# Performance work log

Hardware: AMD Instinct MI355X
Metric: run time of the kernel (lower is better)

## Reference

```python
import jax, jax.numpy as jnp
import numpy as np

F_DIM = 64; HID = 64; HEADS = 2; DH = 32; NG = 4; EPS = 1e-5; SCALE = 8.0  # sqrt(hid_dim)
B = 4; H = 64; W = 64; S = 8; CIN = 64


def _ln(x, g, b):
    mu = x.mean(-1, keepdims=True)
    var = ((x - mu) ** 2).mean(-1, keepdims=True)
    return (x - mu) * jax.lax.rsqrt(var + EPS) * g + b


def _gn(x, g, b):
    # x: [b, C, H, W]; normalize per group over (C/NG, H, W)
    bb, c, hh, ww = x.shape
    xg = x.reshape(bb, NG, -1)
    mu = xg.mean(-1, keepdims=True)
    var = ((xg - mu) ** 2).mean(-1, keepdims=True)
    xn = ((xg - mu) * jax.lax.rsqrt(var + EPS)).reshape(bb, c, hh, ww)
    return xn * g[None, :, None, None] + b[None, :, None, None]


def _mha(xq, xkv, qw, qb, kw, kb, vw, vb, ow, ob):
    # per-head attention with scaling by sqrt(hid_dim) (as in the source)
    q = xq @ qw + qb
    k = xkv @ kw + kb
    v = xkv @ vw + vb
    bb, l, _ = q.shape
    m = k.shape[1]
    qh = q.reshape(bb, l, HEADS, DH)
    kh = k.reshape(bb, m, HEADS, DH)
    vh = v.reshape(bb, m, HEADS, DH)
    s = jnp.einsum('blhd,bmhd->bhlm', qh, kh) / SCALE
    p = jax.nn.softmax(s, axis=-1)
    z = jnp.einsum('bhlm,bmhd->blhd', p, vh).reshape(bb, l, HID)
    return z @ ow + ob


def setup_inputs() -> dict:
    key = jax.random.key(0)
    ks = jax.random.split(key, 34)
    p = lambda k, shp: (jax.random.normal(k, shp, jnp.float32) * 0.02)
    d = {
        'x': jax.random.normal(ks[0], (B, H, W, F_DIM), jnp.float32),
        'slots': jax.random.normal(ks[1], (B, S, CIN), jnp.float32),
        'conv1_w': p(ks[2], (F_DIM, F_DIM)), 'conv1_b': p(ks[3], (F_DIM,)),
        'conv2_w': p(ks[4], (F_DIM, F_DIM)), 'conv2_b': p(ks[5], (F_DIM,)),
        'gn_g': jnp.ones((F_DIM,), jnp.float32), 'gn_b': jnp.zeros((F_DIM,), jnp.float32),
        'ln2_g': jnp.ones((F_DIM,), jnp.float32), 'ln2_b': jnp.zeros((F_DIM,), jnp.float32),
        'ln3_g': jnp.ones((F_DIM,), jnp.float32), 'ln3_b': jnp.zeros((F_DIM,), jnp.float32),
        'ln4_g': jnp.ones((F_DIM,), jnp.float32), 'ln4_b': jnp.zeros((F_DIM,), jnp.float32),
        'sa_qw': p(ks[6], (F_DIM, HID)), 'sa_qb': p(ks[7], (HID,)),
        'sa_kw': p(ks[8], (F_DIM, HID)), 'sa_kb': p(ks[9], (HID,)),
        'sa_vw': p(ks[10], (F_DIM, HID)), 'sa_vb': p(ks[11], (HID,)),
        'sa_ow': p(ks[12], (HID, F_DIM)), 'sa_ob': p(ks[13], (F_DIM,)),
        'ca_qw': p(ks[14], (F_DIM, HID)), 'ca_qb': p(ks[15], (HID,)),
        'ca_kw': p(ks[16], (CIN, HID)), 'ca_kb': p(ks[17], (HID,)),
        'ca_vw': p(ks[18], (CIN, HID)), 'ca_vb': p(ks[19], (HID,)),
        'ca_ow': p(ks[20], (HID, F_DIM)), 'ca_ob': p(ks[21], (F_DIM,)),
        'ff1_w': p(ks[22], (F_DIM, F_DIM)), 'ff1_b': p(ks[23], (F_DIM,)),
    }
    return d


def reference(x, slots, conv1_w, conv1_b, conv2_w, conv2_b, gn_g, gn_b,
              ln2_g, ln2_b, ln3_g, ln3_b, ln4_g, ln4_b,
              sa_qw, sa_qb, sa_kw, sa_kb, sa_vw, sa_vb, sa_ow, sa_ob,
              ca_qw, ca_qb, ca_kw, ca_kb, ca_vw, ca_vb, ca_ow, ca_ob,
              ff1_w, ff1_b):
    b, h, w, f = x.shape
    xc = jnp.transpose(x, (0, 3, 1, 2))               # [b,f,h,w]
    xc = _gn(xc, gn_g, gn_b)
    xc = jnp.einsum('bchw,oc->bohw', xc, conv1_w) + conv1_b[None, :, None, None]
    # faithful to torch: .contiguous().view(b,-1,f) on channels-first layout
    xs = xc.reshape(b, h * w, f)
    # repeat = 1
    xs = jax.nn.gelu(_ln(_mha(xs, xs, sa_qw, sa_qb, sa_kw, sa_kb, sa_vw, sa_vb, sa_ow, sa_ob), ln2_g, ln2_b) + xs, approximate=False)
    xs = _ln(_mha(xs, slots, ca_qw, ca_qb, ca_kw, ca_kb, ca_vw, ca_vb, ca_ow, ca_ob), ln3_g, ln3_b) + xs
    xs = _ln(xs @ ff1_w + ff1_b, ln4_g, ln4_b) + xs
    xo = jnp.transpose(xs.reshape(b, h, w, f), (0, 3, 1, 2))
    xo = jnp.einsum('bchw,oc->bohw', xo, conv2_w) + conv2_b[None, :, None, None]
    return jnp.transpose(xo, (0, 2, 3, 1))
```

## Files before the change

### kernel.cpp

```cpp
#include <hip/hip_runtime.h>
#include <hip/hip_bf16.h>
#include <math.h>

#define NBATCH 4
#define LTOK   4096
#define FD     64
#define KSPLIT 8
#define MBLK   16

typedef __attribute__((ext_vector_type(8))) short short8v;
typedef __attribute__((ext_vector_type(4))) float f32x4;
typedef __attribute__((ext_vector_type(16))) float f32x16;

static __device__ inline uint32_t packbf2(float a, float b) {
    float2 f; f.x = a; f.y = b;
    __hip_bfloat162 h = __float22bfloat162_rn(f);
    uint32_t u; __builtin_memcpy(&u, &h, 4);
    return u;
}
static __device__ inline ushort packbf1(float a) {
    __hip_bfloat16 h = __float2bfloat16(a);
    ushort u; __builtin_memcpy(&u, &h, 2);
    return u;
}
static __device__ inline float gelu_exact(float y) {
    return 0.5f * y * (1.0f + erff(y * 0.70710678118654752f));
}

__global__ void gn_part_kernel(const float* __restrict__ x,
                               float* __restrict__ partS, float* __restrict__ partSS) {
    const int b = blockIdx.x >> 6, c = blockIdx.x & 63;
    const int t = threadIdx.x, l = t & 63, wv = t >> 6;
    const float4* xb = (const float4*)(x + (size_t)b * 262144) + (size_t)c * 1024;
    float s = 0.f, ss = 0.f;
#pragma unroll
    for (int k = 0; k < 4; k++) {
        float4 v = xb[t + 256 * k];
        s += (v.x + v.y) + (v.z + v.w);
        ss += (v.x * v.x + v.y * v.y) + (v.z * v.z + v.w * v.w);
    }
#pragma unroll
    for (int o = 0; o < 4; o++) {
        const int off = (int[]){1, 2, 16, 32}[o];
        s += __shfl_xor(s, off, 64);
        ss += __shfl_xor(ss, off, 64);
    }
    __shared__ float ls_s[4][4], ls_ss[4][4];
    if ((l & 51) == 0) { ls_s[wv][(l >> 2) & 3] = s; ls_ss[wv][(l >> 2) & 3] = ss; }
    __syncthreads();
    if (t < 4) {
        float S = 0.f, SS = 0.f;
#pragma unroll
        for (int w2 = 0; w2 < 4; w2++) { S += ls_s[w2][t]; SS += ls_ss[w2][t]; }
        partS[b * 256 + t * 64 + c] = S;
        partSS[b * 256 + t * 64 + c] = SS;
    }
}

__global__ void gn_conv1_kernel(const float* __restrict__ x,
                                const float* __restrict__ partS, const float* __restrict__ partSS,
                                const float* __restrict__ gg, const float* __restrict__ gb,
                                const float* __restrict__ w, const float* __restrict__ bias,
                                float* __restrict__ out) {
    const int b = blockIdx.x >> 6, i = blockIdx.x & 63;
    const int t = threadIdx.x;
    __shared__ float xn[64][65];
    __shared__ float wsm[64][64];
    __shared__ float sm[4], sr[4];
    {
        float sv = partS[b * 256 + t];
        float ssv = partSS[b * 256 + t];
        for (int o = 32; o; o >>= 1) { sv += __shfl_xor(sv, o, 64); ssv += __shfl_xor(ssv, o, 64); }
        if ((t & 63) == 0) {
            float mean = sv * (1.f / 65536.f);
            float var = ssv * (1.f / 65536.f) - mean * mean;
            sm[t >> 6] = mean;
            sr[t >> 6] = rsqrtf(var + 1e-5f);
        }
    }
    __syncthreads();
    {
        const int j = t >> 2, c0 = (t & 3) * 16, g = c0 >> 4;
        const float mean = sm[g], rstd = sr[g];
        const float* src = x + (((size_t)b * 64 + i) * 64 + j) * 64 + c0;
#pragma unroll
        for (int k = 0; k < 4; k++) {
            float4 v = *(const float4*)(src + 4 * k);
            xn[j][c0 + 4 * k + 0] = (v.x - mean) * rstd * gg[c0 + 4 * k + 0] + gb[c0 + 4 * k + 0];
            xn[j][c0 + 4 * k + 1] = (v.y - mean) * rstd * gg[c0 + 4 * k + 1] + gb[c0 + 4 * k + 1];
            xn[j][c0 + 4 * k + 2] = (v.z - mean) * rstd * gg[c0 + 4 * k + 2] + gb[c0 + 4 * k + 2];
            xn[j][c0 + 4 * k + 3] = (v.w - mean) * rstd * gg[c0 + 4 * k + 3] + gb[c0 + 4 * k + 3];
        }
        const int o = t >> 2, cc0 = (t & 3) * 16;
#pragma unroll
        for (int k = 0; k < 16; k++) wsm[cc0 + k][o] = w[o * 64 + cc0 + k];
    }
    __syncthreads();
    const int jj = t & 63, olo = (t >> 6) * 16;
    float acc[16];
#pragma unroll
    for (int oi = 0; oi < 16; oi++) acc[oi] = bias[olo + oi];
    for (int c = 0; c < 64; c++) {
        float xv = xn[jj][c];
#pragma unroll
        for (int oi = 0; oi < 16; oi++) acc[oi] += xv * wsm[c][olo + oi];
    }
#pragma unroll
    for (int oi = 0; oi < 16; oi++)
        out[((size_t)b * LTOK + (size_t)(olo + oi) * 64 + i) * 64 + jj] = acc[oi];
}

__global__ void qkv_kernel(const float* __restrict__ in,
                           const float* __restrict__ qw, const float* __restrict__ qb,
                           const float* __restrict__ kw, const float* __restrict__ kb,
                           const float* __restrict__ vw, const float* __restrict__ vb,
                           ushort* __restrict__ Qo, ushort* __restrict__ KF, ushort* __restrict__ VF) {
    __shared__ float xt[64][68];
    __shared__ float wt[64][64];
    __shared__ ushort vtr[64 * 72];
    const int t = threadIdx.x;
    const int ph = blockIdx.y;
    const size_t tok0 = (size_t)blockIdx.x * 64;
    const int b = blockIdx.x >> 6;
    const int tokb0 = (blockIdx.x & 63) * 64;
    const int r = t >> 2, cq = t & 3, olo = cq * 16;
    const float* W = (ph == 0) ? qw : (ph == 1) ? kw : vw;
    const float* Bb = (ph == 0) ? qb : (ph == 1) ? kb : vb;
    {
        const float4* src = (const float4*)(in + tok0 * 64) + (size_t)t * 4;
        float4* dst = (float4*)&xt[r][olo];
#pragma unroll
        for (int k = 0; k < 4; k++) dst[k] = src[k];
        const float4* ws2 = (const float4*)W + (size_t)t * 4;
        float4* wd = (float4*)wt + (size_t)t * 4;
#pragma unroll
        for (int k = 0; k < 4; k++) wd[k] = ws2[k];
    }
    __syncthreads();
    float acc[16];
#pragma unroll
    for (int k = 0; k < 4; k++) {
        float4 bv = *(const float4*)(Bb + olo + 4 * k);
        acc[4 * k] = bv.x; acc[4 * k + 1] = bv.y; acc[4 * k + 2] = bv.z; acc[4 * k + 3] = bv.w;
    }
    for (int f = 0; f < 64; f++) {
        float xv = xt[r][f];
#pragma unroll
        for (int oi = 0; oi < 16; oi++) acc[oi] += xv * wt[f][olo + oi];
    }
    if (ph == 0) {
        const float sc = 0.180336880111f;
        uint32_t u[8];
#pragma unroll
        for (int i = 0; i < 8; i++) u[i] = packbf2(acc[2 * i] * sc, acc[2 * i + 1] * sc);
        ushort* op = Qo + (tok0 + r) * 64 + olo;
        *(uint4*)op = make_uint4(u[0], u[1], u[2], u[3]);
        *(uint4*)(op + 8) = make_uint4(u[4], u[5], u[6], u[7]);
    } else if (ph == 1) {
        uint32_t u[8];
#pragma unroll
        for (int i = 0; i < 8; i++) u[i] = packbf2(acc[2 * i], acc[2 * i + 1]);
        const int tokb = tokb0 + r;
        const int m = tokb >> 5, tq = tokb & 31;
        const int hh = cq >> 1, f = cq & 1;
        const int bhh = b * 2 + hh;
        ushort* p0 = KF + ((size_t)(bhh * 128 + m) * 2 + f) * 512;
        *(uint4*)(p0 + tq * 8)        = make_uint4(u[0], u[1], u[2], u[3]);
        *(uint4*)(p0 + (32 + tq) * 8) = make_uint4(u[4], u[5], u[6], u[7]);
    } else {
#pragma unroll
        for (int oi = 0; oi < 16; oi++) vtr[(olo + oi) * 72 + r] = packbf1(acc[oi]);
        __syncthreads();
        const int o = t >> 2, ch = t & 3;
        const int lq2 = o & 31, hh = o >> 5, bhh = b * 2 + hh;
        const int m = (tokb0 >> 5) + (ch >> 1), f = ch & 1;
        uint4 a0 = *(const uint4*)&vtr[o * 72 + ch * 16];
        uint4 a1 = *(const uint4*)&vtr[o * 72 + ch * 16 + 8];
        ushort* p0 = VF + ((size_t)(bhh * 128 + m) * 2 + f) * 512;
        *(uint4*)(p0 + lq2 * 8)        = a0;
        *(uint4*)(p0 + (32 + lq2) * 8) = a1;
    }
}

__global__ __launch_bounds__(256, 4) void flash_mfma(const ushort* __restrict__ Q,
                                                     const ushort* __restrict__ KF,
                                                     const ushort* __restrict__ VF,
                                                     ushort* __restrict__ ZpAll,
                                                     float* __restrict__ Ls) {
    const int qt = blockIdx.x;
    const int bh = blockIdx.y;
    const int ks = blockIdx.z;
    const int b = bh >> 1, h = bh & 1;
    const int t = threadIdx.x;
    const int w = t >> 6, l = t & 63, lq = l & 31, sig = l >> 5;

    const size_t base = (size_t)b * LTOK * 64 + h * 32;
    const int q0 = qt * 256 + w * 64;

    const ushort* qp = Q + base + (size_t)(q0 + lq) * 64 + 8 * sig;
    const short8v qfA0 = *(const short8v*)(qp);
    const short8v qfA1 = *(const short8v*)(qp + 16);
    const short8v qfB0 = *(const short8v*)(qp + 32 * 64);
    const short8v qfB1 = *(const short8v*)(qp + 32 * 64 + 16);

    const ushort* kfp = KF + ((size_t)(bh * 128 + ks * MBLK) * 2) * 512 + l * 8;
    const ushort* vfp = VF + ((size_t)(bh * 128 + ks * MBLK) * 2) * 512 + l * 8;

    f32x16 accA, accB, zero16;
#pragma unroll
    for (int i = 0; i < 16; i++) { accA[i] = 0.f; accB[i] = 0.f; zero16[i] = 0.f; }
    float laccA = 0.f, laccB = 0.f;

    auto mk_aP = [&](const f32x16& st, float& lacc, short8v& aP0v, short8v& aP1v) {
        uint32_t pk[8];
#pragma unroll
        for (int i = 0; i < 8; i++) {
            float p0 = __builtin_amdgcn_exp2f(st[2 * i]);
            float p1 = __builtin_amdgcn_exp2f(st[2 * i + 1]);
            lacc += p0 + p1;
            pk[i] = packbf2(p0, p1);
        }
        uint32_t w0 = pk[0], w2 = pk[2], w1 = pk[1], w3 = pk[3];
        uint32_t x0 = pk[4], x2 = pk[6], x1 = pk[5], x3 = pk[7];
        asm volatile("v_permlane32_swap_b32 %0, %1" : "+v"(w0), "+v"(w2));
        asm volatile("v_permlane32_swap_b32 %0, %1" : "+v"(w1), "+v"(w3));
        asm volatile("v_permlane32_swap_b32 %0, %1" : "+v"(x0), "+v"(x2));
        asm volatile("v_permlane32_swap_b32 %0, %1" : "+v"(x1), "+v"(x3));
        uint4 A0 = make_uint4(w0, w1, w2, w3), A1 = make_uint4(x0, x1, x2, x3);
        __builtin_memcpy(&aP0v, &A0, 16);
        __builtin_memcpy(&aP1v, &A1, 16);
    };

#pragma unroll 4
    for (int m = 0; m < MBLK; m++) {
        const short8v kf0 = *(const short8v*)kfp;
        const short8v kf1 = *(const short8v*)(kfp + 512);
        const short8v vf0 = *(const short8v*)vfp;
        const short8v vf1 = *(const short8v*)(vfp + 512);
        kfp += 1024; vfp += 1024;

        f32x16 st = __builtin_amdgcn_mfma_f32_32x32x16_bf16(kf0, qfA0, zero16, 0, 0, 0);
        st = __builtin_amdgcn_mfma_f32_32x32x16_bf16(kf1, qfA1, st, 0, 0, 0);
        short8v aPA0, aPA1;
        mk_aP(st, laccA, aPA0, aPA1);

        f32x16 st2 = __builtin_amdgcn_mfma_f32_32x32x16_bf16(kf0, qfB0, zero16, 0, 0, 0);
        st2 = __builtin_amdgcn_mfma_f32_32x32x16_bf16(kf1, qfB1, st2, 0, 0, 0);
        short8v aPB0, aPB1;
        mk_aP(st2, laccB, aPB0, aPB1);

        accA = __builtin_amdgcn_mfma_f32_32x32x16_bf16(aPA0, vf0, accA, 0, 0, 0);
        accA = __builtin_amdgcn_mfma_f32_32x32x16_bf16(aPA1, vf1, accA, 0, 0, 0);
        accB = __builtin_amdgcn_mfma_f32_32x32x16_bf16(aPB0, vf0, accB, 0, 0, 0);
        accB = __builtin_amdgcn_mfma_f32_32x32x16_bf16(aPB1, vf1, accB, 0, 0, 0);
    }

    ushort* Zo = ZpAll + (size_t)ks * (NBATCH * LTOK * FD);
#pragma unroll
    for (int r = 0; r < 16; r++) {
        const int qr = q0 + (r & 3) + 8 * (r >> 2) + 4 * sig;
        Zo[base + (size_t)qr * 64 + lq] = packbf1(accA[r]);
        Zo[base + (size_t)(qr + 32) * 64 + lq] = packbf1(accB[r]);
    }
    laccA += __shfl_xor(laccA, 32, 64);
    laccB += __shfl_xor(laccB, 32, 64);
    if (l < 32) {
        Ls[ks * 32768 + bh * 4096 + q0 + lq] = laccA;
        Ls[ks * 32768 + bh * 4096 + q0 + 32 + lq] = laccB;
    }
}

__global__ __launch_bounds__(256) void tail_fused(
    const ushort* __restrict__ ZpAll,
    const float* __restrict__ Ls, const float* __restrict__ xs0,
    const float* __restrict__ slots,
    const float* __restrict__ ckw, const float* __restrict__ ckb,
    const float* __restrict__ cvw, const float* __restrict__ cvb,
    const float* __restrict__ ow, const float* __restrict__ ob,
    const float* __restrict__ g2, const float* __restrict__ b2,
    const float* __restrict__ qw, const float* __restrict__ qb,
    const float* __restrict__ cow, const float* __restrict__ cob,
    const float* __restrict__ g3, const float* __restrict__ b3,
    const float* __restrict__ fw, const float* __restrict__ fb,
    const float* __restrict__ g4, const float* __restrict__ b4,
    const float* __restrict__ cw, const float* __restrict__ cb,
    float* __restrict__ out)
{
    const int t = threadIdx.x;
    const size_t tok0 = (size_t)blockIdx.x * 32;
    const int b = blockIdx.x >> 7;
    const int r = t >> 3, c = t & 7, olo = c * 8;
    __shared__ float xt[32][68];
    __shared__ float wt[64][64];
    __shared__ float kcs[512], vcs[512], sls[512];

    float acc[8], res[8];

    auto stage_w = [&](const float* W) {
#pragma unroll
        for (int k = 0; k < 4; k++)
            ((float4*)wt)[4 * t + k] = ((const float4*)W)[4 * t + k];
    };
    auto stage_x_res = [&]() {
        float4* xd = (float4*)&xt[r][olo];
        xd[0] = make_float4(res[0], res[1], res[2], res[3]);
        xd[1] = make_float4(res[4], res[5], res[6], res[7]);
    };
    auto load8 = [&](float* dst, const float* p) {
        float4 u0 = *(const float4*)(p + olo);
        float4 u1 = *(const float4*)(p + olo + 4);
        dst[0] = u0.x; dst[1] = u0.y; dst[2] = u0.z; dst[3] = u0.w;
        dst[4] = u1.x; dst[5] = u1.y; dst[6] = u1.z; dst[7] = u1.w;
    };
    auto mm = [&](const float* bias) {
        load8(acc, bias);
        for (int f = 0; f < 64; f++) {
            float xv = xt[r][f];
#pragma unroll
            for (int oi = 0; oi < 8; oi++) acc[oi] += xv * wt[f][olo + oi];
        }
    };
    auto ln = [&](const float* gv, const float* bv, bool dogelu) {
        float s1 = 0.f, s2 = 0.f;
#pragma unroll
        for (int oi = 0; oi < 8; oi++) { s1 += acc[oi]; s2 += acc[oi] * acc[oi]; }
#pragma unroll
        for (int o = 1; o <= 4; o <<= 1) {
            s1 += __shfl_xor(s1, o, 64);
            s2 += __shfl_xor(s2, o, 64);
        }
        float mean = s1 * (1.f / 64.f);
        float var = s2 * (1.f / 64.f) - mean * mean;
        float rstd = rsqrtf(var + 1e-5f);
        float gl[8], bl[8];
        load8(gl, gv); load8(bl, bv);
#pragma unroll
        for (int oi = 0; oi < 8; oi++) {
            float y = (acc[oi] - mean) * rstd * gl[oi] + bl[oi] + res[oi];
            res[oi] = dogelu ? gelu_exact(y) : y;
        }
    };

    {
        if (t < 128) ((float4*)sls)[t] = ((const float4*)(slots + (size_t)b * 512))[t];
        float zs[8];
#pragma unroll
        for (int j = 0; j < 8; j++) zs[j] = 0.f;
#pragma unroll
        for (int kb = 0; kb < KSPLIT; kb++) {
            const uint4 u = *(const uint4*)(ZpAll + (size_t)kb * (NBATCH * LTOK * FD)
                                            + tok0 * 64 + (size_t)t * 8);
            const uint32_t arr[4] = {u.x, u.y, u.z, u.w};
#pragma unroll
            for (int j = 0; j < 4; j++) {
                zs[2 * j]     += __uint_as_float(arr[j] << 16);
                zs[2 * j + 1] += __uint_as_float(arr[j] & 0xffff0000u);
            }
        }
        const int hh = olo >> 5;
        const int bh_ = b * 2 + hh;
        const int tokb = (blockIdx.x & 127) * 32 + r;
        float lt = 0.f;
#pragma unroll
        for (int kb = 0; kb < KSPLIT; kb++) lt += Ls[kb * 32768 + bh_ * 4096 + tokb];
        const float inv = 1.0f / lt;
        float4* xd = (float4*)&xt[r][olo];
        xd[0] = make_float4(zs[0] * inv, zs[1] * inv, zs[2] * inv, zs[3] * inv);
        xd[1] = make_float4(zs[4] * inv, zs[5] * inv, zs[6] * inv, zs[7] * inv);
        stage_w(ow);
        float4 r0 = *(const float4*)(xs0 + (tok0 + r) * 64 + olo);
        float4 r1 = *(const float4*)(xs0 + (tok0 + r) * 64 + olo + 4);
        res[0] = r0.x; res[1] = r0.y; res[2] = r0.z; res[3] = r0.w;
        res[4] = r1.x; res[5] = r1.y; res[6] = r1.z; res[7] = r1.w;
    }
    __syncthreads();
    for (int jo = t; jo < 512; jo += 256) {
        const int j = jo >> 6, o = jo & 63;
        float ak = ckb[o], av = cvb[o];
#pragma unroll 8
        for (int c2 = 0; c2 < 64; c2++) {
            float sv = sls[j * 64 + c2];
            ak += sv * ckw[c2 * 64 + o];
            av += sv * cvw[c2 * 64 + o];
        }
        kcs[jo] = ak; vcs[jo] = av;
    }
    mm(ob);
    ln(g2, b2, true);

    __syncthreads();
    stage_x_res();
    stage_w(qw);
    __syncthreads();
    mm(qb);
    {
        float p[8];
        float mx = -3.0e38f;
#pragma unroll
        for (int j = 0; j < 8; j++) {
            float d = 0.f;
#pragma unroll
            for (int i2 = 0; i2 < 8; i2++) d += acc[i2] * kcs[j * 64 + olo + i2];
            d += __shfl_xor(d, 1, 64);
            d += __shfl_xor(d, 2, 64);
            d *= 0.125f;
            p[j] = d;
            mx = fmaxf(mx, d);
        }
        float es = 0.f;
#pragma unroll
        for (int j = 0; j < 8; j++) { p[j] = __expf(p[j] - mx); es += p[j]; }
        float inv = 1.f / es;
#pragma unroll
        for (int oi = 0; oi < 8; oi++) {
            float z = 0.f;
#pragma unroll
            for (int j = 0; j < 8; j++) z += p[j] * vcs[j * 64 + olo + oi];
            acc[oi] = z * inv;
        }
    }

    __syncthreads();
    {
        float4* xd = (float4*)&xt[r][olo];
        xd[0] = make_float4(acc[0], acc[1], acc[2], acc[3]);
        xd[1] = make_float4(acc[4], acc[5], acc[6], acc[7]);
    }
    stage_w(cow);
    __syncthreads();
    mm(cob);
    ln(g3, b3, false);

    __syncthreads();
    stage_x_res();
    stage_w(fw);
    __syncthreads();
    mm(fb);
    ln(g4, b4, false);

    __syncthreads();
    stage_x_res();
    {
        const int o5 = t >> 2, c5 = (t & 3) * 16;
#pragma unroll
        for (int k = 0; k < 16; k++) wt[c5 + k][o5] = cw[o5 * 64 + c5 + k];
    }
    __syncthreads();
    mm(cb);
    float* op = out + (tok0 + r) * 64 + olo;
    *(float4*)op = make_float4(acc[0], acc[1], acc[2], acc[3]);
    *(float4*)(op + 4) = make_float4(acc[4], acc[5], acc[6], acc[7]);
}

extern "C" void kernel_launch(void* const* d_in, const int* in_sizes, int n_in,
                              void* d_out, int out_size, void* d_ws, size_t ws_size,
                              hipStream_t stream) {
    const float* x       = (const float*)d_in[0];
    const float* slots   = (const float*)d_in[1];
    const float* conv1_w = (const float*)d_in[2];
    const float* conv1_b = (const float*)d_in[3];
    const float* conv2_w = (const float*)d_in[4];
    const float* conv2_b = (const float*)d_in[5];
    const float* gn_g    = (const float*)d_in[6];
    const float* gn_b    = (const float*)d_in[7];
    const float* ln2_g   = (const float*)d_in[8];
    const float* ln2_b   = (const float*)d_in[9];
    const float* ln3_g   = (const float*)d_in[10];
    const float* ln3_b   = (const float*)d_in[11];
    const float* ln4_g   = (const float*)d_in[12];
    const float* ln4_b   = (const float*)d_in[13];
    const float* sa_qw   = (const float*)d_in[14];
    const float* sa_qb   = (const float*)d_in[15];
    const float* sa_kw   = (const float*)d_in[16];
    const float* sa_kb   = (const float*)d_in[17];
    const float* sa_vw   = (const float*)d_in[18];
    const float* sa_vb   = (const float*)d_in[19];
    const float* sa_ow   = (const float*)d_in[20];
    const float* sa_ob   = (const float*)d_in[21];
    const float* ca_qw   = (const float*)d_in[22];
    const float* ca_qb   = (const float*)d_in[23];
    const float* ca_kw   = (const float*)d_in[24];
    const float* ca_kb   = (const float*)d_in[25];
    const float* ca_vw   = (const float*)d_in[26];
    const float* ca_vb   = (const float*)d_in[27];
    const float* ca_ow   = (const float*)d_in[28];
    const float* ca_ob   = (const float*)d_in[29];
    const float* ff1_w   = (const float*)d_in[30];
    const float* ff1_b   = (const float*)d_in[31];

    float* ws = (float*)d_ws;
    const size_t NBUF = (size_t)NBATCH * LTOK * FD;
    float* partS  = ws;
    float* partSS = ws + 1024;
    float* A      = ws + 4096;
    ushort* KF    = (ushort*)(A + NBUF);
    ushort* VF    = KF + NBUF;
    ushort* Qb    = VF + NBUF;
    ushort* ZpAll = Qb + NBUF;
    float* Ls     = (float*)(ZpAll + (size_t)KSPLIT * NBUF);

    gn_part_kernel<<<256, 256, 0, stream>>>(x, partS, partSS);
    gn_conv1_kernel<<<256, 256, 0, stream>>>(x, partS, partSS, gn_g, gn_b, conv1_w, conv1_b, A);
    qkv_kernel<<<dim3(256, 3), 256, 0, stream>>>(A, sa_qw, sa_qb, sa_kw, sa_kb, sa_vw, sa_vb, Qb, KF, VF);
    flash_mfma<<<dim3(16, 8, KSPLIT), 256, 0, stream>>>(Qb, KF, VF, ZpAll, Ls);
    tail_fused<<<512, 256, 0, stream>>>(ZpAll, Ls, A, slots,
                                        ca_kw, ca_kb, ca_vw, ca_vb,
                                        sa_ow, sa_ob, ln2_g, ln2_b,
                                        ca_qw, ca_qb, ca_ow, ca_ob, ln3_g, ln3_b,
                                        ff1_w, ff1_b, ln4_g, ln4_b,
                                        conv2_w, conv2_b, (float*)d_out);
}
```

Baseline: 88.25 us.

## Precompute cross-attn slot K/V once, merge QKV phases, widen small kernels

The cross-attention K/V projection of the slots moves out of tail_fused, where all 512 blocks recomputed it, into one extra block of the GN partial-sum kernel that writes it to workspace. The QKV kernel now computes Q, K and V in one block of 512 threads instead of three separate grid-y phases, loading the input tile once. gn_conv1 also goes to 512 threads with 8 outputs per thread. The extra K/V block is serial within one block and may lengthen the first kernel, and the larger blocks raise register and LDS pressure.

```diff
diff --git a/kernel.cpp b/kernel.cpp
--- a/kernel.cpp
+++ b/kernel.cpp
@@ -28,9 +28,28 @@
 }
 
 __global__ void gn_part_kernel(const float* __restrict__ x,
-                               float* __restrict__ partS, float* __restrict__ partSS) {
+                               const float* __restrict__ slots,
+                               const float* __restrict__ ckw, const float* __restrict__ ckb,
+                               const float* __restrict__ cvw, const float* __restrict__ cvb,
+                               float* __restrict__ partS, float* __restrict__ partSS,
+                               float* __restrict__ kvca) {
+    const int t = threadIdx.x;
+    if (blockIdx.x == 256) {
+        __shared__ float sl[2048];
+        for (int i = t; i < 2048; i += 256) sl[i] = slots[i];
+        __syncthreads();
+        for (int idx = t; idx < 4096; idx += 256) {
+            int which = idx >> 11, rem = idx & 2047, bj = rem >> 6, o = rem & 63;
+            const float* W = which ? cvw : ckw;
+            const float* Bb = which ? cvb : ckb;
+            float acc = Bb[o];
+            for (int c = 0; c < 64; c++) acc += sl[bj * 64 + c] * W[c * 64 + o];
+            kvca[idx] = acc;
+        }
+        return;
+    }
     const int b = blockIdx.x >> 6, c = blockIdx.x & 63;
-    const int t = threadIdx.x, l = t & 63, wv = t >> 6;
+    const int l = t & 63, wv = t >> 6;
     const float4* xb = (const float4*)(x + (size_t)b * 262144) + (size_t)c * 1024;
     float s = 0.f, ss = 0.f;
 #pragma unroll
@@ -57,17 +76,18 @@
     }
 }
 
-__global__ void gn_conv1_kernel(const float* __restrict__ x,
-                                const float* __restrict__ partS, const float* __restrict__ partSS,
-                                const float* __restrict__ gg, const float* __restrict__ gb,
-                                const float* __restrict__ w, const float* __restrict__ bias,
-                                float* __restrict__ out) {
+__global__ __launch_bounds__(512) void gn_conv1_kernel(
+    const float* __restrict__ x,
+    const float* __restrict__ partS, const float* __restrict__ partSS,
+    const float* __restrict__ gg, const float* __restrict__ gb,
+    const float* __restrict__ w, const float* __restrict__ bias,
+    float* __restrict__ out) {
     const int b = blockIdx.x >> 6, i = blockIdx.x & 63;
     const int t = threadIdx.x;
     __shared__ float xn[64][65];
     __shared__ float wsm[64][64];
     __shared__ float sm[4], sr[4];
-    {
+    if (t < 256) {
         float sv = partS[b * 256 + t];
         float ssv = partSS[b * 256 + t];
         for (int o = 32; o; o >>= 1) { sv += __shfl_xor(sv, o, 64); ssv += __shfl_xor(ssv, o, 64); }
@@ -80,105 +100,108 @@
     }
     __syncthreads();
     {
-        const int j = t >> 2, c0 = (t & 3) * 16, g = c0 >> 4;
+        const int j = t >> 3, c0 = (t & 7) * 8, g = c0 >> 4;
         const float mean = sm[g], rstd = sr[g];
         const float* src = x + (((size_t)b * 64 + i) * 64 + j) * 64 + c0;
-#pragma unroll
-        for (int k = 0; k < 4; k++) {
-            float4 v = *(const float4*)(src + 4 * k);
-            xn[j][c0 + 4 * k + 0] = (v.x - mean) * rstd * gg[c0 + 4 * k + 0] + gb[c0 + 4 * k + 0];
-            xn[j][c0 + 4 * k + 1] = (v.y - mean) * rstd * gg[c0 + 4 * k + 1] + gb[c0 + 4 * k + 1];
-            xn[j][c0 + 4 * k + 2] = (v.z - mean) * rstd * gg[c0 + 4 * k + 2] + gb[c0 + 4 * k + 2];
-            xn[j][c0 + 4 * k + 3] = (v.w - mean) * rstd * gg[c0 + 4 * k + 3] + gb[c0 + 4 * k + 3];
-        }
-        const int o = t >> 2, cc0 = (t & 3) * 16;
-#pragma unroll
-        for (int k = 0; k < 16; k++) wsm[cc0 + k][o] = w[o * 64 + cc0 + k];
-    }
-    __syncthreads();
-    const int jj = t & 63, olo = (t >> 6) * 16;
-    float acc[16];
-#pragma unroll
-    for (int oi = 0; oi < 16; oi++) acc[oi] = bias[olo + oi];
+        float4 v0 = *(const float4*)src;
+        float4 v1 = *(const float4*)(src + 4);
+        float vv[8] = {v0.x, v0.y, v0.z, v0.w, v1.x, v1.y, v1.z, v1.w};
+#pragma unroll
+        for (int k = 0; k < 8; k++)
+            xn[j][c0 + k] = (vv[k] - mean) * rstd * gg[c0 + k] + gb[c0 + k];
+        const int o = t >> 3, cc0 = (t & 7) * 8;
+#pragma unroll
+        for (int k = 0; k < 8; k++) wsm[cc0 + k][o] = w[o * 64 + cc0 + k];
+    }
+    __syncthreads();
+    const int jj = t & 63, og = t >> 6;
+    const int olo = og * 8;
+    float acc[8];
+#pragma unroll
+    for (int oi = 0; oi < 8; oi++) acc[oi] = bias[olo + oi];
     for (int c = 0; c < 64; c++) {
         float xv = xn[jj][c];
-#pragma unroll
-        for (int oi = 0; oi < 16; oi++) acc[oi] += xv * wsm[c][olo + oi];
-    }
-#pragma unroll
-    for (int oi = 0; oi < 16; oi++)
+        float4 w0 = *(const float4*)&wsm[c][olo];
+        float4 w1 = *(const float4*)&wsm[c][olo + 4];
+        acc[0] += xv * w0.x; acc[1] += xv * w0.y; acc[2] += xv * w0.z; acc[3] += xv * w0.w;
+        acc[4] += xv * w1.x; acc[5] += xv * w1.y; acc[6] += xv * w1.z; acc[7] += xv * w1.w;
+    }
+#pragma unroll
+    for (int oi = 0; oi < 8; oi++)
         out[((size_t)b * LTOK + (size_t)(olo + oi) * 64 + i) * 64 + jj] = acc[oi];
 }
 
-__global__ void qkv_kernel(const float* __restrict__ in,
-                           const float* __restrict__ qw, const float* __restrict__ qb,
-                           const float* __restrict__ kw, const float* __restrict__ kb,
-                           const float* __restrict__ vw, const float* __restrict__ vb,
-                           ushort* __restrict__ Qo, ushort* __restrict__ KF, ushort* __restrict__ VF) {
+__global__ __launch_bounds__(512) void qkv_kernel(
+    const float* __restrict__ in,
+    const float* __restrict__ qw, const float* __restrict__ qb,
+    const float* __restrict__ kw, const float* __restrict__ kb,
+    const float* __restrict__ vw, const float* __restrict__ vb,
+    ushort* __restrict__ Qo, ushort* __restrict__ KF, ushort* __restrict__ VF) {
     __shared__ float xt[64][68];
-    __shared__ float wt[64][64];
+    __shared__ float wq[64][64], wk2[64][64], wv2[64][64];
     __shared__ ushort vtr[64 * 72];
     const int t = threadIdx.x;
-    const int ph = blockIdx.y;
     const size_t tok0 = (size_t)blockIdx.x * 64;
     const int b = blockIdx.x >> 6;
     const int tokb0 = (blockIdx.x & 63) * 64;
-    const int r = t >> 2, cq = t & 3, olo = cq * 16;
-    const float* W = (ph == 0) ? qw : (ph == 1) ? kw : vw;
-    const float* Bb = (ph == 0) ? qb : (ph == 1) ? kb : vb;
-    {
-        const float4* src = (const float4*)(in + tok0 * 64) + (size_t)t * 4;
-        float4* dst = (float4*)&xt[r][olo];
-#pragma unroll
-        for (int k = 0; k < 4; k++) dst[k] = src[k];
-        const float4* ws2 = (const float4*)W + (size_t)t * 4;
-        float4* wd = (float4*)wt + (size_t)t * 4;
-#pragma unroll
-        for (int k = 0; k < 4; k++) wd[k] = ws2[k];
-    }
-    __syncthreads();
-    float acc[16];
-#pragma unroll
-    for (int k = 0; k < 4; k++) {
-        float4 bv = *(const float4*)(Bb + olo + 4 * k);
-        acc[4 * k] = bv.x; acc[4 * k + 1] = bv.y; acc[4 * k + 2] = bv.z; acc[4 * k + 3] = bv.w;
-    }
-    for (int f = 0; f < 64; f++) {
-        float xv = xt[r][f];
-#pragma unroll
-        for (int oi = 0; oi < 16; oi++) acc[oi] += xv * wt[f][olo + oi];
-    }
-    if (ph == 0) {
+    {
+        const float4* src = (const float4*)(in + tok0 * 64) + 2 * t;
+        float* dst = &xt[t >> 3][(t & 7) * 8];
+        *(float4*)dst = src[0];
+        *(float4*)(dst + 4) = src[1];
+        ((float4*)wq)[2 * t] = ((const float4*)qw)[2 * t];
+        ((float4*)wq)[2 * t + 1] = ((const float4*)qw)[2 * t + 1];
+        ((float4*)wk2)[2 * t] = ((const float4*)kw)[2 * t];
+        ((float4*)wk2)[2 * t + 1] = ((const float4*)kw)[2 * t + 1];
+        ((float4*)wv2)[2 * t] = ((const float4*)vw)[2 * t];
+        ((float4*)wv2)[2 * t + 1] = ((const float4*)vw)[2 * t + 1];
+    }
+    __syncthreads();
+    const int r2 = t >> 3, fo = (t & 7) * 8;
+    const int tokb = tokb0 + r2;
+
+    auto proj = [&](const float (*W)[64], const float* Bb, float* acc) {
+        float4 b0 = *(const float4*)(Bb + fo);
+        float4 b1 = *(const float4*)(Bb + fo + 4);
+        acc[0] = b0.x; acc[1] = b0.y; acc[2] = b0.z; acc[3] = b0.w;
+        acc[4] = b1.x; acc[5] = b1.y; acc[6] = b1.z; acc[7] = b1.w;
+        for (int f = 0; f < 64; f++) {
+            float xv = xt[r2][f];
+            float4 w0 = *(const float4*)&W[f][fo];
+            float4 w1 = *(const float4*)&W[f][fo + 4];
+            acc[0] += xv * w0.x; acc[1] += xv * w0.y; acc[2] += xv * w0.z; acc[3] += xv * w0.w;
+            acc[4] += xv * w1.x; acc[5] += xv * w1.y; acc[6] += xv * w1.z; acc[7] += xv * w1.w;
+        }
+    };
+
+    float acc[8];
+    proj(wq, qb, acc);
+    {
         const float sc = 0.180336880111f;
-        uint32_t u[8];
-#pragma unroll
-        for (int i = 0; i < 8; i++) u[i] = packbf2(acc[2 * i] * sc, acc[2 * i + 1] * sc);
-        ushort* op = Qo + (tok0 + r) * 64 + olo;
-        *(uint4*)op = make_uint4(u[0], u[1], u[2], u[3]);
-        *(uint4*)(op + 8) = make_uint4(u[4], u[5], u[6], u[7]);
-    } else if (ph == 1) {
-        uint32_t u[8];
-#pragma unroll
-        for (int i = 0; i < 8; i++) u[i] = packbf2(acc[2 * i], acc[2 * i + 1]);
-        const int tokb = tokb0 + r;
+        uint4 u = make_uint4(packbf2(acc[0] * sc, acc[1] * sc), packbf2(acc[2] * sc, acc[3] * sc),
+                             packbf2(acc[4] * sc, acc[5] * sc), packbf2(acc[6] * sc, acc[7] * sc));
+        *(uint4*)(Qo + (tok0 + r2) * 64 + fo) = u;
+    }
+    proj(wk2, kb, acc);
+    {
+        uint4 u = make_uint4(packbf2(acc[0], acc[1]), packbf2(acc[2], acc[3]),
+                             packbf2(acc[4], acc[5]), packbf2(acc[6], acc[7]));
         const int m = tokb >> 5, tq = tokb & 31;
-        const int hh = cq >> 1, f = cq & 1;
+        const int hh = fo >> 5, rem = fo & 31, ff = rem >> 4, sg = (rem >> 3) & 1;
         const int bhh = b * 2 + hh;
-        ushort* p0 = KF + ((size_t)(bhh * 128 + m) * 2 + f) * 512;
-        *(uint4*)(p0 + tq * 8)        = make_uint4(u[0], u[1], u[2], u[3]);
-        *(uint4*)(p0 + (32 + tq) * 8) = make_uint4(u[4], u[5], u[6], u[7]);
-    } else {
-#pragma unroll
-        for (int oi = 0; oi < 16; oi++) vtr[(olo + oi) * 72 + r] = packbf1(acc[oi]);
-        __syncthreads();
-        const int o = t >> 2, ch = t & 3;
-        const int lq2 = o & 31, hh = o >> 5, bhh = b * 2 + hh;
-        const int m = (tokb0 >> 5) + (ch >> 1), f = ch & 1;
-        uint4 a0 = *(const uint4*)&vtr[o * 72 + ch * 16];
-        uint4 a1 = *(const uint4*)&vtr[o * 72 + ch * 16 + 8];
-        ushort* p0 = VF + ((size_t)(bhh * 128 + m) * 2 + f) * 512;
-        *(uint4*)(p0 + lq2 * 8)        = a0;
-        *(uint4*)(p0 + (32 + lq2) * 8) = a1;
+        *(uint4*)(KF + ((size_t)(bhh * 128 + m) * 2 + ff) * 512 + (sg * 32 + tq) * 8) = u;
+    }
+    proj(wv2, vb, acc);
+#pragma unroll
+    for (int k = 0; k < 8; k++) vtr[(fo + k) * 72 + r2] = packbf1(acc[k]);
+    __syncthreads();
+    {
+        const int hh2 = t >> 8, mrel = (t >> 7) & 1, f2 = (t >> 6) & 1, slot = t & 63;
+        const int sg2 = slot >> 5, idx = slot & 31;
+        const int tl0 = mrel * 32 + f2 * 16 + sg2 * 8;
+        const int m2 = (tokb0 >> 5) + mrel;
+        uint4 a0 = *(const uint4*)&vtr[(hh2 * 32 + idx) * 72 + tl0];
+        *(uint4*)(VF + ((size_t)((b * 2 + hh2) * 128 + m2) * 2 + f2) * 512 + slot * 8) = a0;
     }
 }
 
@@ -273,9 +296,7 @@
 __global__ __launch_bounds__(256) void tail_fused(
     const ushort* __restrict__ ZpAll,
     const float* __restrict__ Ls, const float* __restrict__ xs0,
-    const float* __restrict__ slots,
-    const float* __restrict__ ckw, const float* __restrict__ ckb,
-    const float* __restrict__ cvw, const float* __restrict__ cvb,
+    const float* __restrict__ kvca,
     const float* __restrict__ ow, const float* __restrict__ ob,
     const float* __restrict__ g2, const float* __restrict__ b2,
     const float* __restrict__ qw, const float* __restrict__ qb,
@@ -292,7 +313,7 @@
     const int r = t >> 3, c = t & 7, olo = c * 8;
     __shared__ float xt[32][68];
     __shared__ float wt[64][64];
-    __shared__ float kcs[512], vcs[512], sls[512];
+    __shared__ float kcs[512], vcs[512];
 
     float acc[8], res[8];
 
@@ -342,7 +363,8 @@
     };
 
     {
-        if (t < 128) ((float4*)sls)[t] = ((const float4*)(slots + (size_t)b * 512))[t];
+        if (t < 128) ((float4*)kcs)[t] = ((const float4*)(kvca + (size_t)b * 512))[t];
+        else if (t < 256) ((float4*)vcs)[t - 128] = ((const float4*)(kvca + 2048 + (size_t)b * 512))[t - 128];
         float zs[8];
 #pragma unroll
         for (int j = 0; j < 8; j++) zs[j] = 0.f;
@@ -374,17 +396,6 @@
         res[4] = r1.x; res[5] = r1.y; res[6] = r1.z; res[7] = r1.w;
     }
     __syncthreads();
-    for (int jo = t; jo < 512; jo += 256) {
-        const int j = jo >> 6, o = jo & 63;
-        float ak = ckb[o], av = cvb[o];
-#pragma unroll 8
-        for (int c2 = 0; c2 < 64; c2++) {
-            float sv = sls[j * 64 + c2];
-            ak += sv * ckw[c2 * 64 + o];
-            av += sv * cvw[c2 * 64 + o];
-        }
-        kcs[jo] = ak; vcs[jo] = av;
-    }
     mm(ob);
     ln(g2, b2, true);
 
@@ -492,19 +503,20 @@
     const size_t NBUF = (size_t)NBATCH * LTOK * FD;
     float* partS  = ws;
     float* partSS = ws + 1024;
-    float* A      = ws + 4096;
+    float* kvca   = ws + 2048;
+    float* A      = ws + 8192;
     ushort* KF    = (ushort*)(A + NBUF);
     ushort* VF    = KF + NBUF;
     ushort* Qb    = VF + NBUF;
     ushort* ZpAll = Qb + NBUF;
     float* Ls     = (float*)(ZpAll + (size_t)KSPLIT * NBUF);
 
-    gn_part_kernel<<<256, 256, 0, stream>>>(x, partS, partSS);
-    gn_conv1_kernel<<<256, 256, 0, stream>>>(x, partS, partSS, gn_g, gn_b, conv1_w, conv1_b, A);
-    qkv_kernel<<<dim3(256, 3), 256, 0, stream>>>(A, sa_qw, sa_qb, sa_kw, sa_kb, sa_vw, sa_vb, Qb, KF, VF);
+    gn_part_kernel<<<257, 256, 0, stream>>>(x, slots, ca_kw, ca_kb, ca_vw, ca_vb,
+                                            partS, partSS, kvca);
+    gn_conv1_kernel<<<256, 512, 0, stream>>>(x, partS, partSS, gn_g, gn_b, conv1_w, conv1_b, A);
+    qkv_kernel<<<256, 512, 0, stream>>>(A, sa_qw, sa_qb, sa_kw, sa_kb, sa_vw, sa_vb, Qb, KF, VF);
     flash_mfma<<<dim3(16, 8, KSPLIT), 256, 0, stream>>>(Qb, KF, VF, ZpAll, Ls);
-    tail_fused<<<512, 256, 0, stream>>>(ZpAll, Ls, A, slots,
-                                        ca_kw, ca_kb, ca_vw, ca_vb,
+    tail_fused<<<512, 256, 0, stream>>>(ZpAll, Ls, A, kvca,
                                         sa_ow, sa_ob, ln2_g, ln2_b,
                                         ca_qw, ca_qb, ca_ow, ca_ob, ln3_g, ln3_b,
                                         ff1_w, ff1_b, ln4_g, ln4_b,
```

New measurement: 108.8 us. 23.3% more time.
